# Kernel tuning notes

Hardware: AMD Instinct MI355X
Metric: run time of the kernel (lower is better)

The kernel has to match this reference:

```python
import jax, jax.numpy as jnp
import numpy as np

N = 50000
E = 800000
IN_DIM = 128
HIDDEN = 256
HP = HIDDEN // 3            # 85
HP2 = HIDDEN - 2 * HP       # 86
OUT_DIM = 40


def setup_inputs() -> dict:
    key = jax.random.key(0)
    ks = jax.random.split(key, 10)
    x = jax.random.normal(ks[0], (N, IN_DIM), dtype=jnp.float32)
    edge_index = jax.random.randint(ks[1], (2, E), 0, N, dtype=jnp.int64)
    s = 1.0 / np.sqrt(IN_DIM)
    W0 = jax.random.uniform(ks[2], (IN_DIM, HP), jnp.float32, -s, s)
    b0 = jax.random.uniform(ks[3], (HP,), jnp.float32, -s, s)
    W1 = jax.random.uniform(ks[4], (IN_DIM, HP), jnp.float32, -s, s)
    b1 = jax.random.uniform(ks[5], (HP,), jnp.float32, -s, s)
    W2 = jax.random.uniform(ks[6], (IN_DIM, HP2), jnp.float32, -s, s)
    b2 = jax.random.uniform(ks[7], (HP2,), jnp.float32, -s, s)
    sf = 1.0 / np.sqrt(HIDDEN)
    Wf = jax.random.uniform(ks[8], (HIDDEN, OUT_DIM), jnp.float32, -sf, sf)
    bf = jax.random.uniform(ks[9], (OUT_DIM,), jnp.float32, -sf, sf)
    return {"x": x, "edge_index": edge_index, "W0": W0, "b0": b0,
            "W1": W1, "b1": b1, "W2": W2, "b2": b2, "Wf": Wf, "bf": bf}


def _spmm(row, col, x, n):
    # adj @ x where adj[row[e], col[e]] = 1 : gather neighbor feats, scatter-add to row
    return jax.ops.segment_sum(x[col], row, num_segments=n)


def reference(x, edge_index, W0, b0, W1, b1, W2, b2, Wf, bf):
    n = x.shape[0]
    row, col = edge_index[0], edge_index[1]
    # out-degree of row nodes, clamped to min 1
    deg = jax.ops.segment_sum(jnp.ones((row.shape[0],), x.dtype), row, num_segments=n)
    deg_inv = 1.0 / jnp.maximum(deg, 1.0)
    # hop 0
    h0 = x @ W0 + b0
    # hop 1: (A x) * deg_inv
    ax = _spmm(row, col, x, n)
    h1 = (ax * deg_inv[:, None]) @ W1 + b1
    # hop 2: (A A x) * deg_inv^2
    aax = _spmm(row, col, ax, n)
    h2 = (aax * (deg_inv ** 2)[:, None]) @ W2 + b2
    h = jax.nn.relu(jnp.concatenate([h0, h1, h2], axis=1))
    # dropout inactive in eval mode
    return h @ Wf + bf
```

## Files before the change

### kernel.cpp

```cpp
#include <hip/hip_runtime.h>

#define N_NODES 50000
#define E_EDGES 800000
#define IN_DIM  128
#define OUT_DIM 40
#define NPAD    50176
#define NBKT    196
#define NBLK    256
#define EPB     3125

#define OFF_CNT   0
#define OFF_BASE  50176
#define OFF_DEG   100352
#define OFF_RS    150528
#define OFF_EPACK 200704
#define OFF_SCOL  1000704
#define OFF_WTBF  1800704
#define OFF_WF2T  1819136
#define OFF_BV    1826048
#define OFF_XBF   1826336
#define OFF_AXBF  (OFF_XBF  + NPAD * 64)
#define OFF_AAXBF (OFF_AXBF + NPAD * 64)
#define OFF_H     (OFF_AAXBF + NPAD * 64)
#define OFF_BTOT  (OFF_H + NPAD * 144)
#define OFF_BOFF  (OFF_BTOT + 256)

typedef short bf16x8 __attribute__((ext_vector_type(8)));
typedef float f32x4  __attribute__((ext_vector_type(4)));

__device__ __forceinline__ short f2bf(float f) {
    unsigned u = __float_as_uint(f);
    unsigned r = u + 0x7FFFu + ((u >> 16) & 1u);
    return (short)(r >> 16);
}

__device__ __forceinline__ bf16x8 cvt8(float4 a, float4 b) {
    bf16x8 v;
    v[0] = f2bf(a.x); v[1] = f2bf(a.y); v[2] = f2bf(a.z); v[3] = f2bf(a.w);
    v[4] = f2bf(b.x); v[5] = f2bf(b.y); v[6] = f2bf(b.z); v[7] = f2bf(b.w);
    return v;
}

__device__ __forceinline__ int block_excl_scan_256(int v, int* total_out,
                                                   int* wtot )
{
    const int t = threadIdx.x;
    const int lane = t & 63, wid = t >> 6;
    int sc = v;
    #pragma unroll
    for (int off = 1; off < 64; off <<= 1) {
        int tmp = __shfl_up(sc, off, 64);
        if (lane >= off) sc += tmp;
    }
    if (lane == 63) wtot[wid] = sc;
    __syncthreads();
    if (t == 0) {
        int a = 0;
        #pragma unroll
        for (int w2 = 0; w2 < 4; ++w2) { int tmp = wtot[w2]; wtot[w2] = a; a += tmp; }
        wtot[4] = a;
    }
    __syncthreads();
    *total_out = wtot[4];
    return sc - v + wtot[wid];
}

__global__ __launch_bounds__(256) void hist_coarse_kernel(
    const int* __restrict__ row, int* __restrict__ cnt)
{
    __shared__ int lbin[NBKT];
    const int t   = threadIdx.x;
    const int blk = blockIdx.x;
    if (t < NBKT) lbin[t] = 0;
    __syncthreads();
    const int e0 = blk * EPB;
    for (int i = t; i < EPB; i += 256)
        atomicAdd(&lbin[row[e0 + i] >> 8], 1);
    __syncthreads();
    if (t < NBKT) cnt[t * NBLK + blk] = lbin[t];
}

__global__ __launch_bounds__(256) void scan_local_kernel(
    const int* __restrict__ cnt, int* __restrict__ base,
    int* __restrict__ btot)
{
    __shared__ int wtot[5];
    const int b = blockIdx.x;
    const int t = threadIdx.x;
    int v = cnt[b * NBLK + t];
    int total;
    int excl = block_excl_scan_256(v, &total, wtot);
    base[b * NBLK + t] = excl;
    if (t == 0) btot[b] = total;
}

__global__ __launch_bounds__(256) void scan_small_kernel(
    const int* __restrict__ btot, int* __restrict__ boff)
{
    __shared__ int wtot[5];
    const int t = threadIdx.x;
    int v = (t < NBKT) ? btot[t] : 0;
    int total;
    int excl = block_excl_scan_256(v, &total, wtot);
    if (t < NBKT) boff[t] = excl;
}

__global__ __launch_bounds__(256) void add_offset_kernel(
    int* __restrict__ base, const int* __restrict__ boff)
{
    const int b = blockIdx.x;
    base[b * NBLK + threadIdx.x] += boff[b];
}

__global__ __launch_bounds__(256) void scatter_coarse_kernel(
    const int* __restrict__ row, const int* __restrict__ col,
    const int* __restrict__ base, unsigned int* __restrict__ epack)
{
    __shared__ int lcnt[NBKT];
    __shared__ int lbs[NBKT];
    const int t   = threadIdx.x;
    const int blk = blockIdx.x;
    if (t < NBKT) { lcnt[t] = 0; lbs[t] = base[t * NBLK + blk]; }
    __syncthreads();
    const int e0 = blk * EPB;
    for (int i = t; i < EPB; i += 256) {
        int r = row[e0 + i];
        int c = col[e0 + i];
        int cb = r >> 8;
        int loc = atomicAdd(&lcnt[cb], 1);
        epack[lbs[cb] + loc] = ((unsigned)(r & 255) << 16) | (unsigned)c;
    }
}

__global__ __launch_bounds__(256) void fine_sort_kernel(
    const unsigned int* __restrict__ epack,
    const int* __restrict__ base,
    int* __restrict__ sorted_col,
    int* __restrict__ deg, int* __restrict__ row_start)
{
    __shared__ int lhist[256];
    __shared__ int lbase[256];
    __shared__ int wtot[5];
    const int t  = threadIdx.x;
    const int cb = blockIdx.x;
    const int s  = base[cb * NBLK];
    const int e2 = (cb == NBKT - 1) ? E_EDGES : base[(cb + 1) * NBLK];

    lhist[t] = 0;
    __syncthreads();
    for (int i = s + t; i < e2; i += 256)
        atomicAdd(&lhist[epack[i] >> 16], 1);
    __syncthreads();

    int v = lhist[t];
    int total;
    int excl = block_excl_scan_256(v, &total, wtot);

    int node = cb * 256 + t;
    deg[node]       = v;
    row_start[node] = s + excl;
    lbase[t] = excl;
    __syncthreads();
    lhist[t] = 0;
    __syncthreads();

    for (int i = s + t; i < e2; i += 256) {
        unsigned p = epack[i];
        int rlo = p >> 16;
        int off = atomicAdd(&lhist[rlo], 1);
        sorted_col[s + lbase[rlo] + off] = (int)(p & 0xFFFFu);
    }
}

__global__ __launch_bounds__(256) void convert_x_kernel(
    const float* __restrict__ x, short* __restrict__ xbf)
{
    int idx = blockIdx.x * 256 + threadIdx.x;
    if (idx >= NPAD * 16) return;
    int node = idx >> 4;
    bf16x8 v;
    if (node < N_NODES) {
        const float4* rp = (const float4*)x + (size_t)idx * 2;
        v = cvt8(rp[0], rp[1]);
    } else {
        #pragma unroll
        for (int j = 0; j < 8; ++j) v[j] = 0;
    }
    *(bf16x8*)(xbf + (size_t)idx * 8) = v;
}

__global__ __launch_bounds__(256) void spmm_gather_kernel(
    const short* __restrict__ src,
    const int*   __restrict__ row_start,
    const int*   __restrict__ sorted_col,
    short*       __restrict__ dst)
{
    int node = (blockIdx.x * 256 + threadIdx.x) >> 4;
    int lane = threadIdx.x & 15;
    if (node >= N_NODES) return;
    int s = row_start[node];
    int e = row_start[node + 1];

    float acc[8];
    #pragma unroll
    for (int j = 0; j < 8; ++j) acc[j] = 0.0f;

    for (int i = s; i < e; i += 8) {
        const int nn = e - i;
        int cidx[8];
        #pragma unroll
        for (int j = 0; j < 8; ++j)
            cidx[j] = sorted_col[i + (j < nn ? j : 0)];
        uint4 v[8];
        #pragma unroll
        for (int j = 0; j < 8; ++j)
            v[j] = *(const uint4*)(src + (size_t)cidx[j] * IN_DIM + lane * 8);
        #pragma unroll
        for (int j = 0; j < 8; ++j) {
            if (j < nn) {
                acc[0] += __uint_as_float(v[j].x << 16);
                acc[1] += __uint_as_float(v[j].x & 0xFFFF0000u);
                acc[2] += __uint_as_float(v[j].y << 16);
                acc[3] += __uint_as_float(v[j].y & 0xFFFF0000u);
                acc[4] += __uint_as_float(v[j].z << 16);
                acc[5] += __uint_as_float(v[j].z & 0xFFFF0000u);
                acc[6] += __uint_as_float(v[j].w << 16);
                acc[7] += __uint_as_float(v[j].w & 0xFFFF0000u);
            }
        }
    }
    bf16x8 r;
    #pragma unroll
    for (int j = 0; j < 8; ++j) r[j] = f2bf(acc[j]);
    *(bf16x8*)(dst + (size_t)node * IN_DIM + lane * 8) = r;
}

__global__ __launch_bounds__(256) void setup_weights_kernel(
    const float* __restrict__ W0, const float* __restrict__ b0,
    const float* __restrict__ W1, const float* __restrict__ b1,
    const float* __restrict__ W2, const float* __restrict__ b2,
    const float* __restrict__ Wf,
    short* __restrict__ Wtbf, short* __restrict__ Wf2t,
    float* __restrict__ biasv)
{
    int idx = blockIdx.x * 256 + threadIdx.x;
    if (idx < 288 * 128) {
        int v = idx >> 7, k = idx & 127;
        int s = v / 96, local = v - 96 * s;
        float val = 0.0f;
        if (s == 0 && local < 85)      val = W0[k * 85 + local];
        else if (s == 1 && local < 85) val = W1[k * 85 + local];
        else if (s == 2 && local < 86) val = W2[k * 86 + local];
        Wtbf[idx] = f2bf(val);
    } else if (idx < 288 * 128 + 48 * 288) {
        int j2 = idx - 288 * 128;
        int c = j2 / 288, v = j2 - c * 288;
        int s = v / 96, local = v - 96 * s;
        float val = 0.0f;
        if (c < OUT_DIM && local < ((s == 2) ? 86 : 85))
            val = Wf[(s * 85 + local) * OUT_DIM + c];
        Wf2t[j2] = f2bf(val);
    } else if (idx < 288 * 128 + 48 * 288 + 288) {
        int v = idx - (288 * 128 + 48 * 288);
        int s = v / 96, local = v - 96 * s;
        float val = 0.0f;
        if (s == 0 && local < 85)      val = b0[local];
        else if (s == 1 && local < 85) val = b1[local];
        else if (s == 2 && local < 86) val = b2[local];
        biasv[v] = val;
    }
}

__global__ __launch_bounds__(256) void dense1_mfma_kernel(
    const short* __restrict__ xbf,
    const short* __restrict__ axbf,
    const short* __restrict__ aaxbf,
    const int*   __restrict__ deg,
    const short* __restrict__ Wtbf,
    const float* __restrict__ biasv,
    short* __restrict__ h)
{
    __shared__ short bl[96 * 132];

    const int tid  = threadIdx.x;
    const int w    = tid >> 6;
    const int lane = tid & 63;
    const int il   = lane & 15;
    const int kq   = lane >> 4;
    const int s    = blockIdx.y;
    const int m0   = blockIdx.x * 64 + w * 16;

    #pragma unroll
    for (int j = 0; j < 6; ++j) {
        int idx  = tid + j * 256;
        int brow = idx >> 4;
        int slot = idx & 15;
        uint4 v = *(const uint4*)(Wtbf + (size_t)(s * 96 + brow) * IN_DIM + slot * 8);
        *(uint4*)(bl + brow * 132 + slot * 8) = v;
    }
    __syncthreads();

    const short* __restrict__ src = (s == 0) ? xbf : (s == 1) ? axbf : aaxbf;
    const int arow = m0 + il;

    f32x4 acc[6];
    #pragma unroll
    for (int c = 0; c < 6; ++c)
        #pragma unroll
        for (int q = 0; q < 4; ++q) acc[c][q] = 0.0f;

    #pragma unroll
    for (int kk = 0; kk < 4; ++kk) {
        bf16x8 afrag = *(const bf16x8*)(
            src + (size_t)arow * IN_DIM + kk * 32 + kq * 8);
        #pragma unroll
        for (int c = 0; c < 6; ++c) {
            bf16x8 bfrag = *(const bf16x8*)(
                bl + (c * 16 + il) * 132 + (kk * 4 + kq) * 8);
            acc[c] = __builtin_amdgcn_mfma_f32_16x16x32_bf16(
                afrag, bfrag, acc[c], 0, 0, 0);
        }
    }
    #pragma unroll
    for (int j = 0; j < 4; ++j) {
        int node = m0 + kq * 4 + j;
        float sc = 1.0f;
        if (s) {
            float dv = 1.0f / fmaxf((float)deg[node], 1.0f);
            sc = (s == 1) ? dv : dv * dv;
        }
        #pragma unroll
        for (int c = 0; c < 6; ++c) {
            int vcol = s * 96 + c * 16 + il;
            float hv = fmaf(acc[c][j], sc, biasv[vcol]);
            h[(size_t)node * 288 + vcol] = f2bf(fmaxf(hv, 0.0f));
        }
    }
}

__global__ __launch_bounds__(256) void dense2_mfma_kernel(
    const short* __restrict__ h,
    const short* __restrict__ Wf2t,
    const float* __restrict__ bfin,
    float* __restrict__ out)
{
    __shared__ short bl[16 * 296];

    const int tid  = threadIdx.x;
    const int w    = tid >> 6;
    const int lane = tid & 63;
    const int il   = lane & 15;
    const int kq   = lane >> 4;
    const int cc   = blockIdx.y;
    const int m0   = blockIdx.x * 64 + w * 16;

    #pragma unroll
    for (int j = 0; j < 3; ++j) {
        int idx = tid + j * 256;
        if (idx < 576) {
            int brow = idx / 36;
            int slot = idx - brow * 36;
            uint4 v = *(const uint4*)(Wf2t + (size_t)(cc * 16 + brow) * 288 + slot * 8);
            *(uint4*)(bl + brow * 296 + slot * 8) = v;
        }
    }
    __syncthreads();

    f32x4 acc;
    #pragma unroll
    for (int q = 0; q < 4; ++q) acc[q] = 0.0f;

    #pragma unroll
    for (int kk = 0; kk < 9; ++kk) {
        bf16x8 afrag = *(const bf16x8*)(
            h + (size_t)(m0 + il) * 288 + kk * 32 + kq * 8);
        bf16x8 bfrag = *(const bf16x8*)(
            bl + il * 296 + (kk * 4 + kq) * 8);
        acc = __builtin_amdgcn_mfma_f32_16x16x32_bf16(
            afrag, bfrag, acc, 0, 0, 0);
    }
    int colo = cc * 16 + il;
    if (colo < OUT_DIM) {
        float b = bfin[colo];
        #pragma unroll
        for (int j = 0; j < 4; ++j) {
            int node = m0 + kq * 4 + j;
            if (node < N_NODES)
                out[(size_t)node * OUT_DIM + colo] = acc[j] + b;
        }
    }
}

extern "C" void kernel_launch(void* const* d_in, const int* in_sizes, int n_in,
                              void* d_out, int out_size, void* d_ws, size_t ws_size,
                              hipStream_t stream)
{
    const float* x  = (const float*)d_in[0];
    const int*   ei = (const int*)  d_in[1];
    const float* W0 = (const float*)d_in[2];
    const float* b0 = (const float*)d_in[3];
    const float* W1 = (const float*)d_in[4];
    const float* b1 = (const float*)d_in[5];
    const float* W2 = (const float*)d_in[6];
    const float* b2 = (const float*)d_in[7];
    const float* Wf = (const float*)d_in[8];
    const float* bf = (const float*)d_in[9];
    float* out = (float*)d_out;

    const int* row = ei;
    const int* col = ei + E_EDGES;

    int* wsw = (int*)d_ws;
    int*          cnt        = wsw + OFF_CNT;
    int*          base       = wsw + OFF_BASE;
    int*          deg        = wsw + OFF_DEG;
    int*          row_start  = wsw + OFF_RS;
    unsigned int* epack      = (unsigned int*)(wsw + OFF_EPACK);
    int*          sorted_col = wsw + OFF_SCOL;
    short*        Wtbf       = (short*)(wsw + OFF_WTBF);
    short*        Wf2t       = (short*)(wsw + OFF_WF2T);
    float*        biasv      = (float*)(wsw + OFF_BV);
    short*        xbf        = (short*)(wsw + OFF_XBF);
    short*        axbf       = (short*)(wsw + OFF_AXBF);
    short*        aaxbf      = (short*)(wsw + OFF_AAXBF);
    short*        h          = (short*)(wsw + OFF_H);
    int*          btot       = wsw + OFF_BTOT;
    int*          boff       = wsw + OFF_BOFF;

    dim3 blk(256);
    convert_x_kernel     <<<NPAD * 16 / 256, blk, 0, stream>>>(x, xbf);
    hist_coarse_kernel   <<<NBLK, blk, 0, stream>>>(row, cnt);
    scan_local_kernel    <<<NBKT, blk, 0, stream>>>(cnt, base, btot);
    scan_small_kernel    <<<1, blk, 0, stream>>>(btot, boff);
    add_offset_kernel    <<<NBKT, blk, 0, stream>>>(base, boff);
    scatter_coarse_kernel<<<NBLK, blk, 0, stream>>>(row, col, base, epack);
    fine_sort_kernel     <<<NBKT, blk, 0, stream>>>(epack, base, sorted_col,
                                                    deg, row_start);

    const int sg = (N_NODES * 16 + 255) / 256;
    spmm_gather_kernel<<<sg, blk, 0, stream>>>(xbf,  row_start, sorted_col, axbf);
    spmm_gather_kernel<<<sg, blk, 0, stream>>>(axbf, row_start, sorted_col, aaxbf);

    setup_weights_kernel<<<200, blk, 0, stream>>>(W0, b0, W1, b1, W2, b2, Wf,
                                                  Wtbf, Wf2t, biasv);

    dense1_mfma_kernel<<<dim3(NPAD / 64, 3), blk, 0, stream>>>(
        xbf, axbf, aaxbf, deg, Wtbf, biasv, h);
    dense2_mfma_kernel<<<dim3(NPAD / 64, 3), blk, 0, stream>>>(
        h, Wf2t, bf, out);
}
```

Baseline: 125.5 us.

## Fuse dense layers via LDS h-tile and merge prep/scan kernels

```diff
diff --git a/kernel.cpp b/kernel.cpp
--- a/kernel.cpp
+++ b/kernel.cpp
@@ -21,8 +21,7 @@
 #define OFF_XBF   1826336
 #define OFF_AXBF  (OFF_XBF  + NPAD * 64)
 #define OFF_AAXBF (OFF_AXBF + NPAD * 64)
-#define OFF_H     (OFF_AAXBF + NPAD * 64)
-#define OFF_BTOT  (OFF_H + NPAD * 144)
+#define OFF_BTOT  (OFF_AAXBF + NPAD * 64)
 #define OFF_BOFF  (OFF_BTOT + 256)
 
 typedef short bf16x8 __attribute__((ext_vector_type(8)));
@@ -65,19 +64,69 @@
     return sc - v + wtot[wid];
 }
 
-__global__ __launch_bounds__(256) void hist_coarse_kernel(
-    const int* __restrict__ row, int* __restrict__ cnt)
+__global__ __launch_bounds__(256) void prep_kernel(
+    const float* __restrict__ x, short* __restrict__ xbf,
+    const int* __restrict__ row, int* __restrict__ cnt,
+    const float* __restrict__ W0, const float* __restrict__ b0,
+    const float* __restrict__ W1, const float* __restrict__ b1,
+    const float* __restrict__ W2, const float* __restrict__ b2,
+    const float* __restrict__ Wf,
+    short* __restrict__ Wtbf, short* __restrict__ Wf2t,
+    float* __restrict__ biasv)
 {
     __shared__ int lbin[NBKT];
-    const int t   = threadIdx.x;
-    const int blk = blockIdx.x;
-    if (t < NBKT) lbin[t] = 0;
-    __syncthreads();
-    const int e0 = blk * EPB;
-    for (int i = t; i < EPB; i += 256)
-        atomicAdd(&lbin[row[e0 + i] >> 8], 1);
-    __syncthreads();
-    if (t < NBKT) cnt[t * NBLK + blk] = lbin[t];
+    const int t = threadIdx.x;
+    const int b = blockIdx.x;
+
+    if (b < 3136) {
+        int idx = b * 256 + t;
+        int node = idx >> 4;
+        bf16x8 v;
+        if (node < N_NODES) {
+            const float4* rp = (const float4*)x + (size_t)idx * 2;
+            v = cvt8(rp[0], rp[1]);
+        } else {
+            #pragma unroll
+            for (int j = 0; j < 8; ++j) v[j] = 0;
+        }
+        *(bf16x8*)(xbf + (size_t)idx * 8) = v;
+    } else if (b < 3136 + NBLK) {
+        const int blk = b - 3136;
+        if (t < NBKT) lbin[t] = 0;
+        __syncthreads();
+        const int e0 = blk * EPB;
+        for (int i = t; i < EPB; i += 256)
+            atomicAdd(&lbin[row[e0 + i] >> 8], 1);
+        __syncthreads();
+        if (t < NBKT) cnt[t * NBLK + blk] = lbin[t];
+    } else {
+        int idx = (b - 3392) * 256 + t;
+        if (idx < 288 * 128) {
+            int v = idx >> 7, k = idx & 127;
+            int s = v / 96, local = v - 96 * s;
+            float val = 0.0f;
+            if (s == 0 && local < 85)      val = W0[k * 85 + local];
+            else if (s == 1 && local < 85) val = W1[k * 85 + local];
+            else if (s == 2 && local < 86) val = W2[k * 86 + local];
+            Wtbf[idx] = f2bf(val);
+        } else if (idx < 288 * 128 + 48 * 288) {
+            int j2 = idx - 288 * 128;
+            int c = j2 / 288, v = j2 - c * 288;
+            int s = v / 96, local = v - 96 * s;
+            float val = 0.0f;
+            if (c < OUT_DIM && local < ((s == 2) ? 86 : 85))
+                val = Wf[(s * 85 + local) * OUT_DIM + c];
+            Wf2t[j2] = f2bf(val);
+        } else if (idx < 288 * 128 + 48 * 288 + 288) {
+            int v = idx - (288 * 128 + 48 * 288);
+            int s = v / 96, local = v - 96 * s;
+            float val = 0.0f;
+            if (s == 0 && local < 85)      val = b0[local];
+            else if (s == 1 && local < 85) val = b1[local];
+            else if (s == 2 && local < 86) val = b2[local];
+            biasv[v] = val;
+        }
+    }
 }
 
 __global__ __launch_bounds__(256) void scan_local_kernel(
@@ -94,22 +143,20 @@
     if (t == 0) btot[b] = total;
 }
 
-__global__ __launch_bounds__(256) void scan_small_kernel(
-    const int* __restrict__ btot, int* __restrict__ boff)
+__global__ __launch_bounds__(256) void scan_add_kernel(
+    const int* __restrict__ btot, int* __restrict__ base)
 {
     __shared__ int wtot[5];
+    __shared__ int sh[256];
     const int t = threadIdx.x;
+    const int b = blockIdx.x;
     int v = (t < NBKT) ? btot[t] : 0;
     int total;
     int excl = block_excl_scan_256(v, &total, wtot);
-    if (t < NBKT) boff[t] = excl;
-}
-
-__global__ __launch_bounds__(256) void add_offset_kernel(
-    int* __restrict__ base, const int* __restrict__ boff)
-{
-    const int b = blockIdx.x;
-    base[b * NBLK + threadIdx.x] += boff[b];
+    sh[t] = excl;
+    __syncthreads();
+    int off = sh[b];
+    base[b * NBLK + t] += off;
 }
 
 __global__ __launch_bounds__(256) void scatter_coarse_kernel(
@@ -170,23 +217,6 @@
         int off = atomicAdd(&lhist[rlo], 1);
         sorted_col[s + lbase[rlo] + off] = (int)(p & 0xFFFFu);
     }
-}
-
-__global__ __launch_bounds__(256) void convert_x_kernel(
-    const float* __restrict__ x, short* __restrict__ xbf)
-{
-    int idx = blockIdx.x * 256 + threadIdx.x;
-    if (idx >= NPAD * 16) return;
-    int node = idx >> 4;
-    bf16x8 v;
-    if (node < N_NODES) {
-        const float4* rp = (const float4*)x + (size_t)idx * 2;
-        v = cvt8(rp[0], rp[1]);
-    } else {
-        #pragma unroll
-        for (int j = 0; j < 8; ++j) v[j] = 0;
-    }
-    *(bf16x8*)(xbf + (size_t)idx * 8) = v;
 }
 
 __global__ __launch_bounds__(256) void spmm_gather_kernel(
@@ -235,158 +265,114 @@
     *(bf16x8*)(dst + (size_t)node * IN_DIM + lane * 8) = r;
 }
 
-__global__ __launch_bounds__(256) void setup_weights_kernel(
-    const float* __restrict__ W0, const float* __restrict__ b0,
-    const float* __restrict__ W1, const float* __restrict__ b1,
-    const float* __restrict__ W2, const float* __restrict__ b2,
-    const float* __restrict__ Wf,
-    short* __restrict__ Wtbf, short* __restrict__ Wf2t,
-    float* __restrict__ biasv)
-{
-    int idx = blockIdx.x * 256 + threadIdx.x;
-    if (idx < 288 * 128) {
-        int v = idx >> 7, k = idx & 127;
-        int s = v / 96, local = v - 96 * s;
-        float val = 0.0f;
-        if (s == 0 && local < 85)      val = W0[k * 85 + local];
-        else if (s == 1 && local < 85) val = W1[k * 85 + local];
-        else if (s == 2 && local < 86) val = W2[k * 86 + local];
-        Wtbf[idx] = f2bf(val);
-    } else if (idx < 288 * 128 + 48 * 288) {
-        int j2 = idx - 288 * 128;
-        int c = j2 / 288, v = j2 - c * 288;
-        int s = v / 96, local = v - 96 * s;
-        float val = 0.0f;
-        if (c < OUT_DIM && local < ((s == 2) ? 86 : 85))
-            val = Wf[(s * 85 + local) * OUT_DIM + c];
-        Wf2t[j2] = f2bf(val);
-    } else if (idx < 288 * 128 + 48 * 288 + 288) {
-        int v = idx - (288 * 128 + 48 * 288);
-        int s = v / 96, local = v - 96 * s;
-        float val = 0.0f;
-        if (s == 0 && local < 85)      val = b0[local];
-        else if (s == 1 && local < 85) val = b1[local];
-        else if (s == 2 && local < 86) val = b2[local];
-        biasv[v] = val;
-    }
-}
-
-__global__ __launch_bounds__(256) void dense1_mfma_kernel(
+#define HTS 296
+
+__global__ __launch_bounds__(256) void dense_fused_kernel(
     const short* __restrict__ xbf,
     const short* __restrict__ axbf,
     const short* __restrict__ aaxbf,
     const int*   __restrict__ deg,
     const short* __restrict__ Wtbf,
+    const short* __restrict__ Wf2t,
     const float* __restrict__ biasv,
-    short* __restrict__ h)
-{
-    __shared__ short bl[96 * 132];
+    const float* __restrict__ bfin,
+    float* __restrict__ out)
+{
+    __shared__ short wbuf[96 * 132];
+    __shared__ short htile[64 * HTS];
 
     const int tid  = threadIdx.x;
     const int w    = tid >> 6;
     const int lane = tid & 63;
     const int il   = lane & 15;
     const int kq   = lane >> 4;
-    const int s    = blockIdx.y;
     const int m0   = blockIdx.x * 64 + w * 16;
 
-    #pragma unroll
-    for (int j = 0; j < 6; ++j) {
-        int idx  = tid + j * 256;
-        int brow = idx >> 4;
-        int slot = idx & 15;
-        uint4 v = *(const uint4*)(Wtbf + (size_t)(s * 96 + brow) * IN_DIM + slot * 8);
-        *(uint4*)(bl + brow * 132 + slot * 8) = v;
-    }
-    __syncthreads();
-
-    const short* __restrict__ src = (s == 0) ? xbf : (s == 1) ? axbf : aaxbf;
-    const int arow = m0 + il;
-
-    f32x4 acc[6];
-    #pragma unroll
-    for (int c = 0; c < 6; ++c)
-        #pragma unroll
-        for (int q = 0; q < 4; ++q) acc[c][q] = 0.0f;
-
-    #pragma unroll
-    for (int kk = 0; kk < 4; ++kk) {
-        bf16x8 afrag = *(const bf16x8*)(
-            src + (size_t)arow * IN_DIM + kk * 32 + kq * 8);
-        #pragma unroll
-        for (int c = 0; c < 6; ++c) {
-            bf16x8 bfrag = *(const bf16x8*)(
-                bl + (c * 16 + il) * 132 + (kk * 4 + kq) * 8);
-            acc[c] = __builtin_amdgcn_mfma_f32_16x16x32_bf16(
-                afrag, bfrag, acc[c], 0, 0, 0);
-        }
-    }
+    float dvj[4];
     #pragma unroll
     for (int j = 0; j < 4; ++j) {
         int node = m0 + kq * 4 + j;
-        float sc = 1.0f;
-        if (s) {
-            float dv = 1.0f / fmaxf((float)deg[node], 1.0f);
-            sc = (s == 1) ? dv : dv * dv;
-        }
-        #pragma unroll
-        for (int c = 0; c < 6; ++c) {
-            int vcol = s * 96 + c * 16 + il;
-            float hv = fmaf(acc[c][j], sc, biasv[vcol]);
-            h[(size_t)node * 288 + vcol] = f2bf(fmaxf(hv, 0.0f));
-        }
-    }
-}
-
-__global__ __launch_bounds__(256) void dense2_mfma_kernel(
-    const short* __restrict__ h,
-    const short* __restrict__ Wf2t,
-    const float* __restrict__ bfin,
-    float* __restrict__ out)
-{
-    __shared__ short bl[16 * 296];
-
-    const int tid  = threadIdx.x;
-    const int w    = tid >> 6;
-    const int lane = tid & 63;
-    const int il   = lane & 15;
-    const int kq   = lane >> 4;
-    const int cc   = blockIdx.y;
-    const int m0   = blockIdx.x * 64 + w * 16;
-
-    #pragma unroll
-    for (int j = 0; j < 3; ++j) {
-        int idx = tid + j * 256;
-        if (idx < 576) {
-            int brow = idx / 36;
-            int slot = idx - brow * 36;
-            uint4 v = *(const uint4*)(Wf2t + (size_t)(cc * 16 + brow) * 288 + slot * 8);
-            *(uint4*)(bl + brow * 296 + slot * 8) = v;
-        }
-    }
-    __syncthreads();
-
-    f32x4 acc;
-    #pragma unroll
-    for (int q = 0; q < 4; ++q) acc[q] = 0.0f;
+        dvj[j] = 1.0f / fmaxf((float)deg[node], 1.0f);
+    }
+
+    #pragma unroll
+    for (int s = 0; s < 3; ++s) {
+        #pragma unroll
+        for (int j = 0; j < 6; ++j) {
+            int idx  = tid + j * 256;
+            int brow = idx >> 4;
+            int slot = idx & 15;
+            uint4 v = *(const uint4*)(Wtbf + (size_t)(s * 96 + brow) * IN_DIM + slot * 8);
+            *(uint4*)(wbuf + brow * 132 + slot * 8) = v;
+        }
+        __syncthreads();
+
+        const short* __restrict__ src = (s == 0) ? xbf : (s == 1) ? axbf : aaxbf;
+        const int arow = m0 + il;
+
+        f32x4 acc[6];
+        #pragma unroll
+        for (int c = 0; c < 6; ++c)
+            #pragma unroll
+            for (int q = 0; q < 4; ++q) acc[c][q] = 0.0f;
+
+        #pragma unroll
+        for (int kk = 0; kk < 4; ++kk) {
+            bf16x8 afrag = *(const bf16x8*)(
+                src + (size_t)arow * IN_DIM + kk * 32 + kq * 8);
+            #pragma unroll
+            for (int c = 0; c < 6; ++c) {
+                bf16x8 bfrag = *(const bf16x8*)(
+                    wbuf + (c * 16 + il) * 132 + kk * 32 + kq * 8);
+                acc[c] = __builtin_amdgcn_mfma_f32_16x16x32_bf16(
+                    afrag, bfrag, acc[c], 0, 0, 0);
+            }
+        }
+
+        #pragma unroll
+        for (int j = 0; j < 4; ++j) {
+            int nl = w * 16 + kq * 4 + j;
+            float sc = (s == 0) ? 1.0f : (s == 1) ? dvj[j] : dvj[j] * dvj[j];
+            #pragma unroll
+            for (int c = 0; c < 6; ++c) {
+                int vcol = s * 96 + c * 16 + il;
+                float hv = fmaf(acc[c][j], sc, biasv[vcol]);
+                htile[nl * HTS + vcol] = f2bf(fmaxf(hv, 0.0f));
+            }
+        }
+        __syncthreads();
+    }
+
+    f32x4 acc2[3];
+    #pragma unroll
+    for (int cc = 0; cc < 3; ++cc)
+        #pragma unroll
+        for (int q = 0; q < 4; ++q) acc2[cc][q] = 0.0f;
 
     #pragma unroll
     for (int kk = 0; kk < 9; ++kk) {
         bf16x8 afrag = *(const bf16x8*)(
-            h + (size_t)(m0 + il) * 288 + kk * 32 + kq * 8);
-        bf16x8 bfrag = *(const bf16x8*)(
-            bl + il * 296 + (kk * 4 + kq) * 8);
-        acc = __builtin_amdgcn_mfma_f32_16x16x32_bf16(
-            afrag, bfrag, acc, 0, 0, 0);
-    }
-    int colo = cc * 16 + il;
-    if (colo < OUT_DIM) {
-        float b = bfin[colo];
-        #pragma unroll
-        for (int j = 0; j < 4; ++j) {
-            int node = m0 + kq * 4 + j;
-            if (node < N_NODES)
-                out[(size_t)node * OUT_DIM + colo] = acc[j] + b;
+            htile + (w * 16 + il) * HTS + kk * 32 + kq * 8);
+        #pragma unroll
+        for (int cc = 0; cc < 3; ++cc) {
+            bf16x8 bfrag = *(const bf16x8*)(
+                Wf2t + (size_t)(cc * 16 + il) * 288 + kk * 32 + kq * 8);
+            acc2[cc] = __builtin_amdgcn_mfma_f32_16x16x32_bf16(
+                afrag, bfrag, acc2[cc], 0, 0, 0);
+        }
+    }
+
+    #pragma unroll
+    for (int cc = 0; cc < 3; ++cc) {
+        int colo = cc * 16 + il;
+        if (colo < OUT_DIM) {
+            float b = bfin[colo];
+            #pragma unroll
+            for (int j = 0; j < 4; ++j) {
+                int node = m0 + kq * 4 + j;
+                if (node < N_NODES)
+                    out[(size_t)node * OUT_DIM + colo] = acc2[cc][j] + b;
+            }
         }
     }
 }
@@ -423,16 +409,15 @@
     short*        xbf        = (short*)(wsw + OFF_XBF);
     short*        axbf       = (short*)(wsw + OFF_AXBF);
     short*        aaxbf      = (short*)(wsw + OFF_AAXBF);
-    short*        h          = (short*)(wsw + OFF_H);
     int*          btot       = wsw + OFF_BTOT;
     int*          boff       = wsw + OFF_BOFF;
+    (void)boff; (void)ws_size; (void)in_sizes; (void)n_in; (void)out_size;
 
     dim3 blk(256);
-    convert_x_kernel     <<<NPAD * 16 / 256, blk, 0, stream>>>(x, xbf);
-    hist_coarse_kernel   <<<NBLK, blk, 0, stream>>>(row, cnt);
+    prep_kernel          <<<3136 + NBLK + 200, blk, 0, stream>>>(
+        x, xbf, row, cnt, W0, b0, W1, b1, W2, b2, Wf, Wtbf, Wf2t, biasv);
     scan_local_kernel    <<<NBKT, blk, 0, stream>>>(cnt, base, btot);
-    scan_small_kernel    <<<1, blk, 0, stream>>>(btot, boff);
-    add_offset_kernel    <<<NBKT, blk, 0, stream>>>(base, boff);
+    scan_add_kernel      <<<NBKT, blk, 0, stream>>>(btot, base);
     scatter_coarse_kernel<<<NBLK, blk, 0, stream>>>(row, col, base, epack);
     fine_sort_kernel     <<<NBKT, blk, 0, stream>>>(epack, base, sorted_col,
                                                     deg, row_start);
@@ -441,11 +426,6 @@
     spmm_gather_kernel<<<sg, blk, 0, stream>>>(xbf,  row_start, sorted_col, axbf);
     spmm_gather_kernel<<<sg, blk, 0, stream>>>(axbf, row_start, sorted_col, aaxbf);
 
-    setup_weights_kernel<<<200, blk, 0, stream>>>(W0, b0, W1, b1, W2, b2, Wf,
-                                                  Wtbf, Wf2t, biasv);
-
-    dense1_mfma_kernel<<<dim3(NPAD / 64, 3), blk, 0, stream>>>(
-        xbf, axbf, aaxbf, deg, Wtbf, biasv, h);
-    dense2_mfma_kernel<<<dim3(NPAD / 64, 3), blk, 0, stream>>>(
-        h, Wf2t, bf, out);
-}
+    dense_fused_kernel<<<NPAD / 64, blk, 0, stream>>>(
+        xbf, axbf, aaxbf, deg, Wtbf, Wf2t, biasv, bf, out);
+}
```

Result: faster. 116.4 us, median of 2 (-7.2%).
